# Kernel tuning notes

Hardware: AMD Instinct MI355X
Metric: run time of the kernel (lower is better)

Reference implementation:

```python
import jax, jax.numpy as jnp
import numpy as np


def conv2d(x, w, b, pad):
    y = jax.lax.conv_general_dilated(
        x, w, window_strides=(1, 1), padding=[(pad, pad), (pad, pad)],
        dimension_numbers=('NCHW', 'OIHW', 'NCHW'))
    return y + b[None, :, None, None]


def prelu(x, a):
    # per-channel PReLU, a: [C]
    a = a[None, :, None, None]
    return jnp.where(x > 0, x, a * x)


def setup_inputs() -> dict:
    key = jax.random.key(0)
    ks = jax.random.split(key, 8)
    B, C, H, W = 8, 64, 64, 64
    CTX, SF = 64, 2
    std = 0.02
    inp = {
        'x_low': jax.random.normal(ks[0], (B, C, H, W), jnp.float32),
        'ctx': jax.random.normal(ks[1], (B, CTX, H, W), jnp.float32),
        # ctx_enc: Conv3x3(64->64) + PReLU(64) + Conv3x3(64->32) + PReLU(32)
        'c1_w': jax.random.normal(ks[2], (CTX, CTX, 3, 3), jnp.float32) * std,
        'c1_b': jnp.zeros((CTX,), jnp.float32),
        'p1_a': jnp.full((CTX,), 0.25, jnp.float32),
        'c2_w': jax.random.normal(ks[3], (CTX // 2, CTX, 3, 3), jnp.float32) * std,
        'c2_b': jnp.zeros((CTX // 2,), jnp.float32),
        'p2_a': jnp.full((CTX // 2,), 0.25, jnp.float32),
        # kernel_pred: Conv1x1(32 -> C*9*sf*sf)
        'kp_w': jax.random.normal(ks[4], (C * 9 * SF * SF, CTX // 2, 1, 1), jnp.float32) * std,
        'kp_b': jnp.zeros((C * 9 * SF * SF,), jnp.float32),
    }
    return inp


def upsample_input(inp, mask, sf):
    B, C, H, W = inp.shape
    # mask -> [B, C, 9, sf, sf, H, W], softmax over the 9 kernel taps
    m = jax.nn.softmax(mask.reshape(B, C, 9, sf, sf, H, W), axis=2)
    # replicate-pad and gather 3x3 neighborhoods: neigh [B, C, 9, H, W]
    xp = jnp.pad(inp, ((0, 0), (0, 0), (1, 1), (1, 1)), mode='edge')
    neigh = jnp.stack([xp[:, :, dy:dy + H, dx:dx + W]
                       for dy in range(3) for dx in range(3)], axis=2)
    # weighted sum over kernel taps -> [B, C, sf, sf, H, W]
    out = jnp.einsum('bckpqhw,bckhw->bcpqhw', m, neigh)
    # faithful to torch: permute(0,1,5,3,4,2) then reshape
    out = jnp.transpose(out, (0, 1, 5, 3, 4, 2))
    return out.reshape(B, C, H * sf, W * sf)


def reference(x_low, ctx, c1_w, c1_b, p1_a, c2_w, c2_b, p2_a, kp_w, kp_b):
    SF = 2
    f = prelu(conv2d(ctx, c1_w, c1_b, pad=1), p1_a)
    f = prelu(conv2d(f, c2_w, c2_b, pad=1), p2_a)
    mask = conv2d(f, kp_w, kp_b, pad=0)
    return upsample_input(x_low, mask, SF)
```

## Files before the change

kernel.cpp:

```cpp
#include <hip/hip_runtime.h>


template <int CIN, int COUT, int CPT>
__global__ __launch_bounds__(512, 4) void k_conv3x3(
    const float* __restrict__ x,
    const float* __restrict__ wgt,
    const float* __restrict__ bias,
    const float* __restrict__ alpha,
    float* __restrict__ y)
{
    const int h = blockIdx.x;
    const int b = blockIdx.y;
    __shared__ float lds[3][CIN][66];
    const int t = threadIdx.x;

    for (int idx = t; idx < 3 * CIN * 64; idx += 512) {
        int r  = idx / (CIN * 64);
        int ci = (idx >> 6) % CIN;
        int w  = idx & 63;
        int hh = h + r - 1;
        float v = 0.f;
        if (hh >= 0 && hh < 64)
            v = x[((b * CIN + ci) * 64 + hh) * 64 + w];
        lds[r][ci][w + 1] = v;
    }
    if (t < 3 * CIN) {
        int r = t / CIN, ci = t % CIN;
        lds[r][ci][0]  = 0.f;
        lds[r][ci][65] = 0.f;
    }
    __syncthreads();

    const int w   = t & 63;
    const int cg  = __builtin_amdgcn_readfirstlane(t >> 6);
    const int co0 = cg * CPT;

    float acc[CPT];
#pragma unroll
    for (int i = 0; i < CPT; ++i) acc[i] = bias[co0 + i];

    for (int ci = 0; ci < CIN; ++ci) {
        float v[3][3];
#pragma unroll
        for (int ky = 0; ky < 3; ++ky) {
            v[ky][0] = lds[ky][ci][w];
            v[ky][1] = lds[ky][ci][w + 1];
            v[ky][2] = lds[ky][ci][w + 2];
        }
#pragma unroll
        for (int co = 0; co < CPT; ++co) {
            const float* wp = &wgt[((co0 + co) * CIN + ci) * 9];
            float a = acc[co];
            a = fmaf(wp[0], v[0][0], a);
            a = fmaf(wp[1], v[0][1], a);
            a = fmaf(wp[2], v[0][2], a);
            a = fmaf(wp[3], v[1][0], a);
            a = fmaf(wp[4], v[1][1], a);
            a = fmaf(wp[5], v[1][2], a);
            a = fmaf(wp[6], v[2][0], a);
            a = fmaf(wp[7], v[2][1], a);
            a = fmaf(wp[8], v[2][2], a);
            acc[co] = a;
        }
    }

#pragma unroll
    for (int co = 0; co < CPT; ++co) {
        float a  = acc[co];
        float al = alpha[co0 + co];
        float o  = (a > 0.f) ? a : al * a;
        y[((b * COUT + co0 + co) * 64 + h) * 64 + w] = o;
    }
}

__global__ __launch_bounds__(512, 4) void k_upsample(
    const float* __restrict__ f2,
    const float* __restrict__ kpw,
    const float* __restrict__ kpb,
    const float* __restrict__ xlow,
    float* __restrict__ out)
{
    const int cq = blockIdx.x;
    const int w  = blockIdx.y;
    const int b  = blockIdx.z;
    __shared__ float F[32][64];
    __shared__ float Xl[32][3][64];
    const int t = threadIdx.x;

    for (int idx = t; idx < 32 * 64; idx += 512) {
        int ci = idx >> 6, h = idx & 63;
        F[ci][h] = f2[((b * 32 + ci) * 64 + h) * 64 + w];
    }
    for (int idx = t; idx < 32 * 3 * 64; idx += 512) {
        int h = idx & 63, dx = (idx >> 6) % 3, ci = idx / 192;
        int ww = min(max(w + dx - 1, 0), 63);
        Xl[ci][dx][h] = xlow[((b * 64 + cq * 32 + ci) * 64 + h) * 64 + ww];
    }
    __syncthreads();

    const int h  = t & 63;
    const int cg = __builtin_amdgcn_readfirstlane(t >> 6);

    float fu[32];
#pragma unroll
    for (int ci = 0; ci < 32; ++ci) fu[ci] = F[ci][h];

    const int hm = max(h - 1, 0), hp = min(h + 1, 63);

    for (int cc = 0; cc < 4; ++cc) {
        const int c  = cq * 32 + cg * 4 + cc;
        const int cl = cg * 4 + cc;
        const float4* wp4 = (const float4*)(kpw + c * 36 * 32);
        const float*  bp  = kpb + c * 36;

#pragma unroll
        for (int q = 0; q < 2; ++q) {
            float o2[2];
#pragma unroll
            for (int p = 0; p < 2; ++p) {
                const int pq = p * 2 + q;
                float acc[9];
#pragma unroll
                for (int k = 0; k < 9; ++k) acc[k] = bp[k * 4 + pq];
#pragma unroll
                for (int ci4 = 0; ci4 < 8; ++ci4) {
                    float f0 = fu[ci4 * 4 + 0], f1 = fu[ci4 * 4 + 1];
                    float f2v = fu[ci4 * 4 + 2], f3 = fu[ci4 * 4 + 3];
#pragma unroll
                    for (int k = 0; k < 9; ++k) {
                        float4 wv = wp4[(k * 4 + pq) * 8 + ci4];
                        acc[k] = fmaf(wv.x, f0,
                                 fmaf(wv.y, f1,
                                 fmaf(wv.z, f2v,
                                 fmaf(wv.w, f3, acc[k]))));
                    }
                }
                float m = acc[0];
#pragma unroll
                for (int k = 1; k < 9; ++k) m = fmaxf(m, acc[k]);
                float s = 0.f, ov = 0.f;
#pragma unroll
                for (int k = 0; k < 9; ++k) {
                    const int dy = k / 3, dx = k % 3;
                    const int hh = (dy == 0) ? hm : (dy == 1 ? h : hp);
                    float e = __expf(acc[k] - m);
                    s += e;
                    ov = fmaf(e, Xl[cl][dx][hh], ov);
                }
                o2[p] = ov / s;
            }
            *(float2*)&out[((b * 64 + c) * 128 + (2 * w + q)) * 128 + 2 * h] =
                make_float2(o2[0], o2[1]);
        }
    }
}

extern "C" void kernel_launch(void* const* d_in, const int* in_sizes, int n_in,
                              void* d_out, int out_size, void* d_ws, size_t ws_size,
                              hipStream_t stream) {
    (void)in_sizes; (void)n_in; (void)out_size; (void)ws_size;
    const float* x_low = (const float*)d_in[0];
    const float* ctx   = (const float*)d_in[1];
    const float* c1_w  = (const float*)d_in[2];
    const float* c1_b  = (const float*)d_in[3];
    const float* p1_a  = (const float*)d_in[4];
    const float* c2_w  = (const float*)d_in[5];
    const float* c2_b  = (const float*)d_in[6];
    const float* p2_a  = (const float*)d_in[7];
    const float* kp_w  = (const float*)d_in[8];
    const float* kp_b  = (const float*)d_in[9];
    float* out = (float*)d_out;

    float* f1 = (float*)d_ws;
    float* f2 = f1 + 8 * 64 * 64 * 64;

    k_conv3x3<64, 64, 8><<<dim3(64, 8), 512, 0, stream>>>(ctx, c1_w, c1_b, p1_a, f1);
    k_conv3x3<64, 32, 4><<<dim3(64, 8), 512, 0, stream>>>(f1, c2_w, c2_b, p2_a, f2);
    k_upsample<<<dim3(2, 64, 8), 512, 0, stream>>>(f2, kp_w, kp_b, x_low, out);
}
```

Before: 309.1 us.

## Drop LDS staging in 3x3 convs and split output channels across blocks

The 3x3 conv kernels no longer stage three input rows into shared memory with a barrier. Each thread now reads its 3x3 neighbourhood straight from global memory, with boundary checks done in registers. The grid gains a dimension that splits output channels across two 256-thread blocks, which doubles the block count and is meant to raise occupancy and remove the sync and LDS cost. In exchange, input rows are re-read from global memory or cache by both channel halves and for each neighbouring tap.

```diff
diff --git a/kernel.cpp b/kernel.cpp
--- a/kernel.cpp
+++ b/kernel.cpp
@@ -2,50 +2,41 @@
 
 
 template <int CIN, int COUT, int CPT>
-__global__ __launch_bounds__(512, 4) void k_conv3x3(
+__global__ __launch_bounds__(256) void k_conv3x3g(
     const float* __restrict__ x,
     const float* __restrict__ wgt,
     const float* __restrict__ bias,
     const float* __restrict__ alpha,
     float* __restrict__ y)
 {
-    const int h = blockIdx.x;
-    const int b = blockIdx.y;
-    __shared__ float lds[3][CIN][66];
+    const int s = blockIdx.x;
+    const int h = blockIdx.y;
+    const int b = blockIdx.z;
     const int t = threadIdx.x;
-
-    for (int idx = t; idx < 3 * CIN * 64; idx += 512) {
-        int r  = idx / (CIN * 64);
-        int ci = (idx >> 6) % CIN;
-        int w  = idx & 63;
-        int hh = h + r - 1;
-        float v = 0.f;
-        if (hh >= 0 && hh < 64)
-            v = x[((b * CIN + ci) * 64 + hh) * 64 + w];
-        lds[r][ci][w + 1] = v;
-    }
-    if (t < 3 * CIN) {
-        int r = t / CIN, ci = t % CIN;
-        lds[r][ci][0]  = 0.f;
-        lds[r][ci][65] = 0.f;
-    }
-    __syncthreads();
-
-    const int w   = t & 63;
-    const int cg  = __builtin_amdgcn_readfirstlane(t >> 6);
-    const int co0 = cg * CPT;
+    const int w  = t & 63;
+    const int cg = __builtin_amdgcn_readfirstlane(t >> 6);
+    const int co0 = (s * 4 + cg) * CPT;
 
     float acc[CPT];
 #pragma unroll
     for (int i = 0; i < CPT; ++i) acc[i] = bias[co0 + i];
 
+    const bool w0 = (w > 0), w1 = (w < 63);
+    const float* xp = x + ((size_t)(b * CIN) * 64 + h) * 64 + w;
+
     for (int ci = 0; ci < CIN; ++ci) {
         float v[3][3];
 #pragma unroll
-        for (int ky = 0; ky < 3; ++ky) {
-            v[ky][0] = lds[ky][ci][w];
-            v[ky][1] = lds[ky][ci][w + 1];
-            v[ky][2] = lds[ky][ci][w + 2];
+        for (int r = 0; r < 3; ++r) {
+            const int hh = h + r - 1;
+            if (hh >= 0 && hh < 64) {
+                const float* p = xp + (r - 1) * 64;
+                v[r][0] = w0 ? p[-1] : 0.f;
+                v[r][1] = p[0];
+                v[r][2] = w1 ? p[1] : 0.f;
+            } else {
+                v[r][0] = 0.f; v[r][1] = 0.f; v[r][2] = 0.f;
+            }
         }
 #pragma unroll
         for (int co = 0; co < CPT; ++co) {
@@ -62,6 +53,7 @@
             a = fmaf(wp[8], v[2][2], a);
             acc[co] = a;
         }
+        xp += 4096;
     }
 
 #pragma unroll
@@ -174,7 +166,7 @@
     float* f1 = (float*)d_ws;
     float* f2 = f1 + 8 * 64 * 64 * 64;
 
-    k_conv3x3<64, 64, 8><<<dim3(64, 8), 512, 0, stream>>>(ctx, c1_w, c1_b, p1_a, f1);
-    k_conv3x3<64, 32, 4><<<dim3(64, 8), 512, 0, stream>>>(f1, c2_w, c2_b, p2_a, f2);
+    k_conv3x3g<64, 64, 8><<<dim3(2, 64, 8), 256, 0, stream>>>(ctx, c1_w, c1_b, p1_a, f1);
+    k_conv3x3g<64, 32, 4><<<dim3(2, 64, 8), 256, 0, stream>>>(f1, c2_w, c2_b, p2_a, f2);
     k_upsample<<<dim3(2, 64, 8), 512, 0, stream>>>(f2, kp_w, kp_b, x_low, out);
 }
```

Result: slower. 324.3 us (+4.9%).
